# Performance work log

Measured on AMD Instinct MI355X. Metric: run time of the kernel, lower is better.

The kernel has to match this reference:

```python
import math
import jax, jax.numpy as jnp
import numpy as np

S, M, B, D, H = 256, 256, 8, 512, 8
HD = D // H
K = S + M  # key_len


def setup_inputs() -> dict:
    key = jax.random.key(0)
    ks = jax.random.split(key, 10)
    x = jax.random.normal(ks[0], (S, B, D), jnp.float32)
    memory = jax.random.normal(ks[1], (M, B, D), jnp.float32)
    rel_pos = jax.random.normal(ks[2], (K, D), jnp.float32)
    # causal mask: True means masked (key position after query position)
    q_pos = jnp.arange(S)[:, None] + M  # (S,1)
    k_pos = jnp.arange(K)[None, :]     # (1,K)
    attn_mask = jnp.broadcast_to(k_pos > q_pos, (B, S, K))
    scale = 1.0 / math.sqrt(D)
    Wq = jax.random.normal(ks[3], (D, D), jnp.float32) * scale
    Wk = jax.random.normal(ks[4], (D, D), jnp.float32) * scale
    Wv = jax.random.normal(ks[5], (D, D), jnp.float32) * scale
    Wr = jax.random.normal(ks[6], (D, D), jnp.float32) * scale
    Wo = jax.random.normal(ks[7], (D, D), jnp.float32) * scale
    u_bias = jax.random.normal(ks[8], (H, HD), jnp.float32) * 0.02
    v_bias = jax.random.normal(ks[9], (H, HD), jnp.float32) * 0.02
    return {"x": x, "memory": memory, "rel_pos": rel_pos, "attn_mask": attn_mask,
            "Wq": Wq, "Wk": Wk, "Wv": Wv, "Wr": Wr, "Wo": Wo,
            "u_bias": u_bias, "v_bias": v_bias}


def reference(x, memory, rel_pos, attn_mask, Wq, Wk, Wv, Wr, Wo, u_bias, v_bias):
    mem = jax.lax.stop_gradient(memory)
    kv = jnp.concatenate([mem, x], axis=0)  # (K, B, D)
    # projections (torch Linear: y = x @ W.T)
    q = (x @ Wq.T).reshape(S, B, H, HD).transpose(1, 2, 0, 3)   # (B,H,S,HD)
    k = (kv @ Wk.T).reshape(K, B, H, HD).transpose(1, 2, 0, 3)  # (B,H,K,HD)
    v = (kv @ Wv.T).reshape(K, B, H, HD).transpose(1, 2, 0, 3)  # (B,H,K,HD)
    r = (rel_pos[:K] @ Wr.T).reshape(K, H, HD)                  # (K,H,HD)
    # relative index gather
    q_pos = jnp.arange(S)[:, None] + M
    k_pos = jnp.arange(K)[None, :]
    rel_idx = jnp.clip(q_pos - k_pos, 0, K - 1)  # (S,K)
    r_qk = r[rel_idx]                            # (S,K,H,HD)
    qk = jnp.einsum('bhqd,bhkd->bhqk', q, k)
    qr = jnp.einsum('bhqd,qkhd->bhqk', q, r_qk)
    uk = jnp.einsum('hd,bhkd->bhk', u_bias, k)[:, :, None, :]
    vr = jnp.einsum('hd,qkhd->hqk', v_bias, r_qk)[None]
    scores = (qk + qr + uk + vr) / math.sqrt(HD)  # (B,H,S,K)
    scores = jnp.where(attn_mask[:, None, :, :], -jnp.inf, scores)
    weights = jax.nn.softmax(scores, axis=-1)
    y = jnp.einsum('bhqk,bhkd->bhqd', weights, v)
    y = y.transpose(2, 0, 1, 3).reshape(S, B, D)
    return y @ Wo.T
```

## Files before the change

### kernel.cpp

```cpp
#include <hip/hip_runtime.h>
#include <math.h>

constexpr int S_  = 256;
constexpr int Mm  = 256;
constexpr int Bb  = 8;
constexpr int Dd  = 512;
constexpr int Hh  = 8;
constexpr int HDd = 64;
constexpr int Kk  = 512;

typedef unsigned short u16;
typedef short bf16x8 __attribute__((ext_vector_type(8)));
typedef float f32x4  __attribute__((ext_vector_type(4)));

constexpr int LROW = 72;
constexpr int QSTR = 520;

__device__ __forceinline__ u16 f2b(float f) {
  union { float f; unsigned int u; } v; v.f = f;
  unsigned int u = v.u + 0x7fffu + ((v.u >> 16) & 1u);
  return (u16)(u >> 16);
}
__device__ __forceinline__ float b2f(u16 b) {
  union { unsigned int u; float f; } v; v.u = ((unsigned int)b) << 16;
  return v.f;
}

__device__ __forceinline__ void stage_bf16(u16* dst, const u16* __restrict__ src,
                                           int ld, int tid) {
  const int r = tid >> 3, c = (tid & 7) * 8;
  *(int4*)(dst + r * LROW + c)        = *(const int4*)(src + (size_t)r * ld + c);
  *(int4*)(dst + (r + 32) * LROW + c) = *(const int4*)(src + (size_t)(r + 32) * ld + c);
}
__device__ __forceinline__ void stage_f32(u16* dst, const float* __restrict__ src,
                                          int ld, int tid, int nrow32) {
  const int r = tid >> 3, c = (tid & 7) * 8;
  for (int hh = 0; hh < nrow32; ++hh) {
    const float4 a = *(const float4*)(src + (size_t)(r + 32 * hh) * ld + c);
    const float4 b = *(const float4*)(src + (size_t)(r + 32 * hh) * ld + c + 4);
    union { u16 u[8]; int4 v; } p;
    p.u[0] = f2b(a.x); p.u[1] = f2b(a.y); p.u[2] = f2b(a.z); p.u[3] = f2b(a.w);
    p.u[4] = f2b(b.x); p.u[5] = f2b(b.y); p.u[6] = f2b(b.z); p.u[7] = f2b(b.w);
    *(int4*)(dst + (r + 32 * hh) * LROW + c) = p.v;
  }
}

__device__ __forceinline__ void mfma_step(const u16* As, const u16* Bs,
                                          f32x4 (&acc)[4], int wave, int lane) {
  const int r16 = lane & 15, q8 = (lane >> 4) * 8;
#pragma unroll
  for (int ks = 0; ks < 64; ks += 32) {
    const bf16x8 a = *(const bf16x8*)(As + (wave * 16 + r16) * LROW + ks + q8);
#pragma unroll
    for (int nb = 0; nb < 4; ++nb) {
      const bf16x8 b = *(const bf16x8*)(Bs + (nb * 16 + r16) * LROW + ks + q8);
      acc[nb] = __builtin_amdgcn_mfma_f32_16x16x32_bf16(a, b, acc[nb], 0, 0, 0);
    }
  }
}

__global__ __launch_bounds__(256) void k_proj(const float* __restrict__ x,
                                              const float* __restrict__ mem,
                                              const float* __restrict__ rel,
                                              const float* __restrict__ Wq,
                                              const float* __restrict__ Wk,
                                              const float* __restrict__ Wv,
                                              const float* __restrict__ Wr,
                                              const float* __restrict__ ub,
                                              const float* __restrict__ vb,
                                              u16* __restrict__ qu,
                                              u16* __restrict__ qv,
                                              u16* __restrict__ kb,
                                              u16* __restrict__ vT,
                                              u16* __restrict__ rT) {
  __shared__ u16 As[128 * LROW], Bs[64 * LROW];
  const int tid = threadIdx.x, wave = tid >> 6, lane = tid & 63;
  const int r16 = lane & 15, q8 = (lane >> 4) * 8, rq = (lane >> 4) * 4;
  const int bid = blockIdx.x;
  int kind, mt, nt;
  const float *A, *B;
  if (bid < 128)      { kind = 0; int t = bid;       mt = t >> 3; nt = t & 7; B = Wq; }
  else if (bid < 384) { kind = 1; int t = bid - 128; mt = t >> 3; nt = t & 7; B = Wk; }
  else if (bid < 640) { kind = 2; int t = bid - 384; mt = t >> 3; nt = t & 7; B = Wv; }
  else                { kind = 3; int t = bid - 640; mt = t >> 3; nt = t & 7; B = Wr; }
  const int m0 = mt * 128, n0 = nt * 64;
  if (kind == 0)      A = x + (size_t)m0 * Dd;
  else if (kind == 3) A = rel + (size_t)m0 * Dd;
  else                A = (m0 < Mm * Bb) ? mem + (size_t)m0 * Dd
                                         : x + (size_t)(m0 - Mm * Bb) * Dd;
  B += (size_t)n0 * Dd;

  f32x4 acc[2][4];
#pragma unroll
  for (int mi = 0; mi < 2; ++mi)
#pragma unroll
    for (int nb = 0; nb < 4; ++nb) acc[mi][nb] = (f32x4){0.f, 0.f, 0.f, 0.f};

  for (int k0 = 0; k0 < Dd; k0 += 64) {
    stage_f32(As, A + k0, Dd, tid, 4);
    stage_f32(Bs, B + k0, Dd, tid, 2);
    __syncthreads();
#pragma unroll
    for (int ks = 0; ks < 64; ks += 32) {
      bf16x8 a[2];
#pragma unroll
      for (int mi = 0; mi < 2; ++mi)
        a[mi] = *(const bf16x8*)(As + (wave * 32 + mi * 16 + r16) * LROW + ks + q8);
#pragma unroll
      for (int nb = 0; nb < 4; ++nb) {
        const bf16x8 bb = *(const bf16x8*)(Bs + (nb * 16 + r16) * LROW + ks + q8);
#pragma unroll
        for (int mi = 0; mi < 2; ++mi)
          acc[mi][nb] = __builtin_amdgcn_mfma_f32_16x16x32_bf16(a[mi], bb, acc[mi][nb], 0, 0, 0);
      }
    }
    __syncthreads();
  }

  const int h = n0 >> 6;
  if (kind == 0) {
#pragma unroll
    for (int nb = 0; nb < 4; ++nb) {
      const int hd = nb * 16 + r16, n = n0 + hd;
      const float u = ub[n], v = vb[n];
#pragma unroll
      for (int mi = 0; mi < 2; ++mi)
#pragma unroll
        for (int r = 0; r < 4; ++r) {
          const int m = m0 + wave * 32 + mi * 16 + rq + r;
          const int s = m >> 3, b = m & 7;
          const size_t d = ((size_t)(b * Hh + h) * S_ + s) * HDd + hd;
          qu[d] = f2b(acc[mi][nb][r] + u);
          qv[d] = f2b(acc[mi][nb][r] + v);
        }
    }
  } else if (kind == 1) {
#pragma unroll
    for (int nb = 0; nb < 4; ++nb) {
      const int hd = nb * 16 + r16;
#pragma unroll
      for (int mi = 0; mi < 2; ++mi)
#pragma unroll
        for (int r = 0; r < 4; ++r) {
          const int m = m0 + wave * 32 + mi * 16 + rq + r;
          const int pos = m >> 3, b = m & 7;
          kb[((size_t)(b * Hh + h) * Kk + pos) * HDd + hd] = f2b(acc[mi][nb][r]);
        }
    }
  } else if (kind == 2) {
#pragma unroll
    for (int nb = 0; nb < 4; ++nb) {
      const int hd = nb * 16 + r16;
#pragma unroll
      for (int mi = 0; mi < 2; ++mi)
#pragma unroll
        for (int r = 0; r < 4; ++r) {
          const int m = m0 + wave * 32 + mi * 16 + rq + r;
          const int pos = m >> 3, b = m & 7;
          vT[((size_t)(b * Hh + h) * HDd + hd) * Kk + pos] = f2b(acc[mi][nb][r]);
        }
    }
  } else {
#pragma unroll
    for (int nb = 0; nb < 4; ++nb) {
      const int hd = nb * 16 + r16;
#pragma unroll
      for (int mi = 0; mi < 2; ++mi)
#pragma unroll
        for (int r = 0; r < 4; ++r) {
          const int j = m0 + wave * 32 + mi * 16 + rq + r;
          rT[((size_t)h * Kk + j) * HDd + hd] = f2b(acc[mi][nb][r]);
        }
    }
  }
}

__global__ __launch_bounds__(256) void k_attn(const u16* __restrict__ qu,
                                              const u16* __restrict__ qv,
                                              const u16* __restrict__ kb,
                                              const u16* __restrict__ vT,
                                              const u16* __restrict__ rT,
                                              u16* __restrict__ y) {
  extern __shared__ u16 lds[];
  u16* QRP = lds;
  u16* Bs  = lds + 64 * QSTR;
  const int tid = threadIdx.x, wave = tid >> 6, lane = tid & 63;
  const int q0 = blockIdx.x * 64, bh = blockIdx.y, h = bh & 7, b = bh >> 3;
  const int ntiles = (q0 >> 6) + 5;
  const int col = lane & 15, rq = (lane >> 4) * 4;
  const int r16 = lane & 15, q8 = (lane >> 4) * 8;

  const u16* qvp = qv + ((size_t)bh * S_ + q0 + wave * 16 + r16) * HDd;
  const bf16x8 av0 = *(const bf16x8*)(qvp + q8);
  const bf16x8 av1 = *(const bf16x8*)(qvp + 32 + q8);
#pragma unroll
  for (int jt = 0; jt < 8; ++jt) if (jt < ntiles) {
    stage_bf16(Bs, rT + ((size_t)h * Kk + jt * 64) * HDd, HDd, tid);
    __syncthreads();
    f32x4 c[4];
#pragma unroll
    for (int i = 0; i < 4; ++i) c[i] = (f32x4){0.f, 0.f, 0.f, 0.f};
#pragma unroll
    for (int ks = 0; ks < 64; ks += 32) {
      const bf16x8 a = ks ? av1 : av0;
#pragma unroll
      for (int nb = 0; nb < 4; ++nb) {
        const bf16x8 bb = *(const bf16x8*)(Bs + (nb * 16 + r16) * LROW + ks + q8);
        c[nb] = __builtin_amdgcn_mfma_f32_16x16x32_bf16(a, bb, c[nb], 0, 0, 0);
      }
    }
#pragma unroll
    for (int nb = 0; nb < 4; ++nb)
#pragma unroll
      for (int r = 0; r < 4; ++r)
        QRP[(wave * 16 + rq + r) * QSTR + jt * 64 + nb * 16 + col] = f2b(c[nb][r]);
    __syncthreads();
  }

  const u16* qup = qu + ((size_t)bh * S_ + q0 + wave * 16 + r16) * HDd;
  const bf16x8 au0 = *(const bf16x8*)(qup + q8);
  const bf16x8 au1 = *(const bf16x8*)(qup + 32 + q8);
  f32x4 sc[8][4];
#pragma unroll
  for (int kt = 0; kt < 8; ++kt) if (kt < ntiles) {
    stage_bf16(Bs, kb + ((size_t)bh * Kk + kt * 64) * HDd, HDd, tid);
    __syncthreads();
#pragma unroll
    for (int i = 0; i < 4; ++i) sc[kt][i] = (f32x4){0.f, 0.f, 0.f, 0.f};
#pragma unroll
    for (int ks = 0; ks < 64; ks += 32) {
      const bf16x8 a = ks ? au1 : au0;
#pragma unroll
      for (int nb = 0; nb < 4; ++nb) {
        const bf16x8 bb = *(const bf16x8*)(Bs + (nb * 16 + r16) * LROW + ks + q8);
        sc[kt][nb] = __builtin_amdgcn_mfma_f32_16x16x32_bf16(a, bb, sc[kt][nb], 0, 0, 0);
      }
    }
    __syncthreads();
  }

  float mx[4] = {-INFINITY, -INFINITY, -INFINITY, -INFINITY};
#pragma unroll
  for (int kt = 0; kt < 8; ++kt) if (kt < ntiles) {
#pragma unroll
    for (int nb = 0; nb < 4; ++nb) {
      const int kk = kt * 64 + nb * 16 + col;
#pragma unroll
      for (int r = 0; r < 4; ++r) {
        const int ql = wave * 16 + rq + r;
        const int q  = q0 + ql;
        float v;
        if (kk <= q + Mm) {
          const float qr = b2f(QRP[ql * QSTR + (q + Mm - kk)]);
          v = (sc[kt][nb][r] + qr) * 0.125f;
        } else {
          v = -INFINITY;
        }
        sc[kt][nb][r] = v;
        mx[r] = fmaxf(mx[r], v);
      }
    }
  }
#pragma unroll
  for (int r = 0; r < 4; ++r)
#pragma unroll
    for (int off = 1; off < 16; off <<= 1) mx[r] = fmaxf(mx[r], __shfl_xor(mx[r], off));
  float sum[4] = {0.f, 0.f, 0.f, 0.f};
#pragma unroll
  for (int kt = 0; kt < 8; ++kt) if (kt < ntiles)
#pragma unroll
    for (int nb = 0; nb < 4; ++nb)
#pragma unroll
      for (int r = 0; r < 4; ++r) {
        const float p = __expf(sc[kt][nb][r] - mx[r]);
        sc[kt][nb][r] = p;
        sum[r] += p;
      }
#pragma unroll
  for (int r = 0; r < 4; ++r)
#pragma unroll
    for (int off = 1; off < 16; off <<= 1) sum[r] += __shfl_xor(sum[r], off);
  float inv[4];
#pragma unroll
  for (int r = 0; r < 4; ++r) inv[r] = 1.0f / sum[r];

#pragma unroll
  for (int kt = 0; kt < 8; ++kt) if (kt < ntiles)
#pragma unroll
    for (int nb = 0; nb < 4; ++nb)
#pragma unroll
      for (int r = 0; r < 4; ++r)
        QRP[(wave * 16 + rq + r) * QSTR + kt * 64 + nb * 16 + col] =
            f2b(sc[kt][nb][r] * inv[r]);
  __syncthreads();

  f32x4 o[4];
#pragma unroll
  for (int i = 0; i < 4; ++i) o[i] = (f32x4){0.f, 0.f, 0.f, 0.f};
#pragma unroll
  for (int kt = 0; kt < 8; ++kt) if (kt < ntiles) {
    stage_bf16(Bs, vT + (size_t)bh * HDd * Kk + kt * 64, Kk, tid);
    __syncthreads();
#pragma unroll
    for (int ks = 0; ks < 64; ks += 32) {
      const bf16x8 a = *(const bf16x8*)(QRP + (wave * 16 + r16) * QSTR + kt * 64 + ks + q8);
#pragma unroll
      for (int nb = 0; nb < 4; ++nb) {
        const bf16x8 bv = *(const bf16x8*)(Bs + (nb * 16 + r16) * LROW + ks + q8);
        o[nb] = __builtin_amdgcn_mfma_f32_16x16x32_bf16(a, bv, o[nb], 0, 0, 0);
      }
    }
    __syncthreads();
  }
#pragma unroll
  for (int nb = 0; nb < 4; ++nb) {
    const int hd = nb * 16 + col;
#pragma unroll
    for (int r = 0; r < 4; ++r) {
      const int q = q0 + wave * 16 + rq + r;
      y[((size_t)q * Bb + b) * Dd + h * HDd + hd] = f2b(o[nb][r]);
    }
  }
}

__global__ __launch_bounds__(256) void k_out(const u16* __restrict__ y,
                                             const float* __restrict__ Wo,
                                             float* __restrict__ out) {
  __shared__ u16 As[64 * LROW], Bs[64 * LROW];
  const int tid = threadIdx.x, wave = tid >> 6, lane = tid & 63;
  const int n0 = blockIdx.x * 64, m0 = blockIdx.y * 64;
  f32x4 acc[4];
#pragma unroll
  for (int i = 0; i < 4; ++i) acc[i] = (f32x4){0.f, 0.f, 0.f, 0.f};
  for (int k0 = 0; k0 < Dd; k0 += 64) {
    stage_bf16(As, y + (size_t)m0 * Dd + k0, Dd, tid);
    stage_f32(Bs, Wo + (size_t)n0 * Dd + k0, Dd, tid, 2);
    __syncthreads();
    mfma_step(As, Bs, acc, wave, lane);
    __syncthreads();
  }
  const int col = lane & 15, rq = (lane >> 4) * 4;
#pragma unroll
  for (int nb = 0; nb < 4; ++nb) {
    const int n = n0 + nb * 16 + col;
#pragma unroll
    for (int r = 0; r < 4; ++r) {
      const int m = m0 + wave * 16 + rq + r;
      out[(size_t)m * Dd + n] = acc[nb][r];
    }
  }
}

extern "C" void kernel_launch(void* const* d_in, const int* in_sizes, int n_in,
                              void* d_out, int out_size, void* d_ws, size_t ws_size,
                              hipStream_t stream) {
  const float* x    = (const float*)d_in[0];
  const float* mem  = (const float*)d_in[1];
  const float* rel  = (const float*)d_in[2];
  const float* Wq = (const float*)d_in[4];
  const float* Wk = (const float*)d_in[5];
  const float* Wv = (const float*)d_in[6];
  const float* Wr = (const float*)d_in[7];
  const float* Wo = (const float*)d_in[8];
  const float* ub = (const float*)d_in[9];
  const float* vb = (const float*)d_in[10];
  float* out = (float*)d_out;

  u16* qu = (u16*)d_ws;
  u16* qv = qu + 1048576;
  u16* kb = qv + 1048576;
  u16* vT = kb + 2097152;
  u16* rT = vT + 2097152;
  u16* yb = rT + 262144;

  constexpr int ATTN_LDS = (64 * QSTR + 64 * LROW) * (int)sizeof(u16);
  (void)hipFuncSetAttribute((const void*)k_attn,
                            hipFuncAttributeMaxDynamicSharedMemorySize, ATTN_LDS);

  k_proj<<<dim3(672),   dim3(256), 0,        stream>>>(x, mem, rel, Wq, Wk, Wv, Wr,
                                                       ub, vb, qu, qv, kb, vT, rT);
  k_attn<<<dim3(4, 64), dim3(256), ATTN_LDS, stream>>>(qu, qv, kb, vT, rT, yb);
  k_out <<<dim3(8, 32), dim3(256), 0,        stream>>>(yb, Wo, out);
}
```

Before: 149.9 us.

## Double-buffer LDS staging in attention and output projection kernels

Merges the three attention phases (relative-position scores, QK scores, PV) into one 24-step loop. Each step prefetches the next tile into registers while computing on the current LDS buffer, halving barriers per tile. The output projection GEMM gets the same register-prefetch double buffering. The attention loop now always processes all 8 key tiles, dropping the causal tile-skipping, which adds work for early query blocks.

```diff
diff --git a/kernel.cpp b/kernel.cpp
--- a/kernel.cpp
+++ b/kernel.cpp
@@ -183,138 +183,159 @@
                                               u16* __restrict__ y) {
   extern __shared__ u16 lds[];
   u16* QRP = lds;
-  u16* Bs  = lds + 64 * QSTR;
+  u16* Bs0 = lds + 64 * QSTR;
+  u16* Bs1 = Bs0 + 64 * LROW;
   const int tid = threadIdx.x, wave = tid >> 6, lane = tid & 63;
   const int q0 = blockIdx.x * 64, bh = blockIdx.y, h = bh & 7, b = bh >> 3;
-  const int ntiles = (q0 >> 6) + 5;
-  const int col = lane & 15, rq = (lane >> 4) * 4;
-  const int r16 = lane & 15, q8 = (lane >> 4) * 8;
+  const int r16 = lane & 15, q8 = (lane >> 4) * 8, rq = (lane >> 4) * 4;
+  const int sr = tid >> 3, scg = (tid & 7) * 8;
 
   const u16* qvp = qv + ((size_t)bh * S_ + q0 + wave * 16 + r16) * HDd;
   const bf16x8 av0 = *(const bf16x8*)(qvp + q8);
   const bf16x8 av1 = *(const bf16x8*)(qvp + 32 + q8);
-#pragma unroll
-  for (int jt = 0; jt < 8; ++jt) if (jt < ntiles) {
-    stage_bf16(Bs, rT + ((size_t)h * Kk + jt * 64) * HDd, HDd, tid);
-    __syncthreads();
-    f32x4 c[4];
-#pragma unroll
-    for (int i = 0; i < 4; ++i) c[i] = (f32x4){0.f, 0.f, 0.f, 0.f};
-#pragma unroll
-    for (int ks = 0; ks < 64; ks += 32) {
-      const bf16x8 a = ks ? av1 : av0;
-#pragma unroll
-      for (int nb = 0; nb < 4; ++nb) {
-        const bf16x8 bb = *(const bf16x8*)(Bs + (nb * 16 + r16) * LROW + ks + q8);
-        c[nb] = __builtin_amdgcn_mfma_f32_16x16x32_bf16(a, bb, c[nb], 0, 0, 0);
-      }
-    }
-#pragma unroll
-    for (int nb = 0; nb < 4; ++nb)
-#pragma unroll
-      for (int r = 0; r < 4; ++r)
-        QRP[(wave * 16 + rq + r) * QSTR + jt * 64 + nb * 16 + col] = f2b(c[nb][r]);
-    __syncthreads();
-  }
-
   const u16* qup = qu + ((size_t)bh * S_ + q0 + wave * 16 + r16) * HDd;
   const bf16x8 au0 = *(const bf16x8*)(qup + q8);
   const bf16x8 au1 = *(const bf16x8*)(qup + 32 + q8);
+
+  const u16* rbase = rT + (size_t)h * Kk * HDd;
+  const u16* kbase = kb + (size_t)bh * Kk * HDd;
+  const u16* vbase = vT + (size_t)bh * HDd * Kk;
+
   f32x4 sc[8][4];
-#pragma unroll
-  for (int kt = 0; kt < 8; ++kt) if (kt < ntiles) {
-    stage_bf16(Bs, kb + ((size_t)bh * Kk + kt * 64) * HDd, HDd, tid);
+  f32x4 o[4];
+#pragma unroll
+  for (int nb = 0; nb < 4; ++nb) o[nb] = (f32x4){0.f, 0.f, 0.f, 0.f};
+  float mx[4]  = {-INFINITY, -INFINITY, -INFINITY, -INFINITY};
+
+  *(int4*)(Bs0 + sr * LROW + scg) =
+      *(const int4*)(rbase + (size_t)sr * HDd + scg);
+  *(int4*)(Bs0 + (sr + 32) * LROW + scg) =
+      *(const int4*)(rbase + (size_t)(sr + 32) * HDd + scg);
+  __syncthreads();
+
+#pragma unroll
+  for (int j = 0; j < 24; ++j) {
+    int4 L0, L1;
+    if (j < 23) {
+      const int jn = j + 1;
+      const u16* s;
+      int ld;
+      if (jn < 8)       { s = rbase + (size_t)(jn * 64) * HDd;       ld = HDd; }
+      else if (jn < 16) { s = kbase + (size_t)((jn - 8) * 64) * HDd; ld = HDd; }
+      else              { s = vbase + (jn - 16) * 64;                ld = Kk;  }
+      L0 = *(const int4*)(s + (size_t)sr * ld + scg);
+      L1 = *(const int4*)(s + (size_t)(sr + 32) * ld + scg);
+    }
+    const u16* buf = (j & 1) ? Bs1 : Bs0;
+
+    if (j < 8) {
+      f32x4 c4[4];
+#pragma unroll
+      for (int nb = 0; nb < 4; ++nb) c4[nb] = (f32x4){0.f, 0.f, 0.f, 0.f};
+#pragma unroll
+      for (int ks = 0; ks < 64; ks += 32) {
+        const bf16x8 a = ks ? av1 : av0;
+#pragma unroll
+        for (int nb = 0; nb < 4; ++nb) {
+          const bf16x8 bb = *(const bf16x8*)(buf + (nb * 16 + r16) * LROW + ks + q8);
+          c4[nb] = __builtin_amdgcn_mfma_f32_16x16x32_bf16(a, bb, c4[nb], 0, 0, 0);
+        }
+      }
+#pragma unroll
+      for (int nb = 0; nb < 4; ++nb)
+#pragma unroll
+        for (int r = 0; r < 4; ++r)
+          QRP[(wave * 16 + rq + r) * QSTR + j * 64 + nb * 16 + r16] = f2b(c4[nb][r]);
+    } else if (j < 16) {
+      const int t = j - 8;
+#pragma unroll
+      for (int nb = 0; nb < 4; ++nb) sc[t][nb] = (f32x4){0.f, 0.f, 0.f, 0.f};
+#pragma unroll
+      for (int ks = 0; ks < 64; ks += 32) {
+        const bf16x8 a = ks ? au1 : au0;
+#pragma unroll
+        for (int nb = 0; nb < 4; ++nb) {
+          const bf16x8 bb = *(const bf16x8*)(buf + (nb * 16 + r16) * LROW + ks + q8);
+          sc[t][nb] = __builtin_amdgcn_mfma_f32_16x16x32_bf16(a, bb, sc[t][nb], 0, 0, 0);
+        }
+      }
+      if (j == 15) {
+#pragma unroll
+        for (int kt = 0; kt < 8; ++kt)
+#pragma unroll
+          for (int nb = 0; nb < 4; ++nb) {
+            const int kk = kt * 64 + nb * 16 + r16;
+#pragma unroll
+            for (int r = 0; r < 4; ++r) {
+              const int ql = wave * 16 + rq + r;
+              const int q  = q0 + ql;
+              float v;
+              if (kk <= q + Mm) {
+                const float qr = b2f(QRP[ql * QSTR + (q + Mm - kk)]);
+                v = (sc[kt][nb][r] + qr) * 0.125f;
+              } else {
+                v = -INFINITY;
+              }
+              sc[kt][nb][r] = v;
+              mx[r] = fmaxf(mx[r], v);
+            }
+          }
+#pragma unroll
+        for (int r = 0; r < 4; ++r)
+#pragma unroll
+          for (int off = 1; off < 16; off <<= 1)
+            mx[r] = fmaxf(mx[r], __shfl_xor(mx[r], off));
+        float sum[4] = {0.f, 0.f, 0.f, 0.f};
+#pragma unroll
+        for (int kt = 0; kt < 8; ++kt)
+#pragma unroll
+          for (int nb = 0; nb < 4; ++nb)
+#pragma unroll
+            for (int r = 0; r < 4; ++r) {
+              const float p = __expf(sc[kt][nb][r] - mx[r]);
+              sc[kt][nb][r] = p;
+              sum[r] += p;
+            }
+#pragma unroll
+        for (int r = 0; r < 4; ++r)
+#pragma unroll
+          for (int off = 1; off < 16; off <<= 1) sum[r] += __shfl_xor(sum[r], off);
+        float inv[4];
+#pragma unroll
+        for (int r = 0; r < 4; ++r) inv[r] = 1.0f / sum[r];
+#pragma unroll
+        for (int kt = 0; kt < 8; ++kt)
+#pragma unroll
+          for (int nb = 0; nb < 4; ++nb)
+#pragma unroll
+            for (int r = 0; r < 4; ++r)
+              QRP[(wave * 16 + rq + r) * QSTR + kt * 64 + nb * 16 + r16] =
+                  f2b(sc[kt][nb][r] * inv[r]);
+      }
+    } else {
+      const int t = j - 16;
+#pragma unroll
+      for (int ks = 0; ks < 64; ks += 32) {
+        const bf16x8 a = *(const bf16x8*)(QRP + (wave * 16 + r16) * QSTR + t * 64 + ks + q8);
+#pragma unroll
+        for (int nb = 0; nb < 4; ++nb) {
+          const bf16x8 bb = *(const bf16x8*)(buf + (nb * 16 + r16) * LROW + ks + q8);
+          o[nb] = __builtin_amdgcn_mfma_f32_16x16x32_bf16(a, bb, o[nb], 0, 0, 0);
+        }
+      }
+    }
+
+    if (j < 23) {
+      u16* d = ((j + 1) & 1) ? Bs1 : Bs0;
+      *(int4*)(d + sr * LROW + scg)        = L0;
+      *(int4*)(d + (sr + 32) * LROW + scg) = L1;
+    }
     __syncthreads();
-#pragma unroll
-    for (int i = 0; i < 4; ++i) sc[kt][i] = (f32x4){0.f, 0.f, 0.f, 0.f};
-#pragma unroll
-    for (int ks = 0; ks < 64; ks += 32) {
-      const bf16x8 a = ks ? au1 : au0;
-#pragma unroll
-      for (int nb = 0; nb < 4; ++nb) {
-        const bf16x8 bb = *(const bf16x8*)(Bs + (nb * 16 + r16) * LROW + ks + q8);
-        sc[kt][nb] = __builtin_amdgcn_mfma_f32_16x16x32_bf16(a, bb, sc[kt][nb], 0, 0, 0);
-      }
-    }
-    __syncthreads();
-  }
-
-  float mx[4] = {-INFINITY, -INFINITY, -INFINITY, -INFINITY};
-#pragma unroll
-  for (int kt = 0; kt < 8; ++kt) if (kt < ntiles) {
-#pragma unroll
-    for (int nb = 0; nb < 4; ++nb) {
-      const int kk = kt * 64 + nb * 16 + col;
-#pragma unroll
-      for (int r = 0; r < 4; ++r) {
-        const int ql = wave * 16 + rq + r;
-        const int q  = q0 + ql;
-        float v;
-        if (kk <= q + Mm) {
-          const float qr = b2f(QRP[ql * QSTR + (q + Mm - kk)]);
-          v = (sc[kt][nb][r] + qr) * 0.125f;
-        } else {
-          v = -INFINITY;
-        }
-        sc[kt][nb][r] = v;
-        mx[r] = fmaxf(mx[r], v);
-      }
-    }
-  }
-#pragma unroll
-  for (int r = 0; r < 4; ++r)
-#pragma unroll
-    for (int off = 1; off < 16; off <<= 1) mx[r] = fmaxf(mx[r], __shfl_xor(mx[r], off));
-  float sum[4] = {0.f, 0.f, 0.f, 0.f};
-#pragma unroll
-  for (int kt = 0; kt < 8; ++kt) if (kt < ntiles)
-#pragma unroll
-    for (int nb = 0; nb < 4; ++nb)
-#pragma unroll
-      for (int r = 0; r < 4; ++r) {
-        const float p = __expf(sc[kt][nb][r] - mx[r]);
-        sc[kt][nb][r] = p;
-        sum[r] += p;
-      }
-#pragma unroll
-  for (int r = 0; r < 4; ++r)
-#pragma unroll
-    for (int off = 1; off < 16; off <<= 1) sum[r] += __shfl_xor(sum[r], off);
-  float inv[4];
-#pragma unroll
-  for (int r = 0; r < 4; ++r) inv[r] = 1.0f / sum[r];
-
-#pragma unroll
-  for (int kt = 0; kt < 8; ++kt) if (kt < ntiles)
-#pragma unroll
-    for (int nb = 0; nb < 4; ++nb)
-#pragma unroll
-      for (int r = 0; r < 4; ++r)
-        QRP[(wave * 16 + rq + r) * QSTR + kt * 64 + nb * 16 + col] =
-            f2b(sc[kt][nb][r] * inv[r]);
-  __syncthreads();
-
-  f32x4 o[4];
-#pragma unroll
-  for (int i = 0; i < 4; ++i) o[i] = (f32x4){0.f, 0.f, 0.f, 0.f};
-#pragma unroll
-  for (int kt = 0; kt < 8; ++kt) if (kt < ntiles) {
-    stage_bf16(Bs, vT + (size_t)bh * HDd * Kk + kt * 64, Kk, tid);
-    __syncthreads();
-#pragma unroll
-    for (int ks = 0; ks < 64; ks += 32) {
-      const bf16x8 a = *(const bf16x8*)(QRP + (wave * 16 + r16) * QSTR + kt * 64 + ks + q8);
-#pragma unroll
-      for (int nb = 0; nb < 4; ++nb) {
-        const bf16x8 bv = *(const bf16x8*)(Bs + (nb * 16 + r16) * LROW + ks + q8);
-        o[nb] = __builtin_amdgcn_mfma_f32_16x16x32_bf16(a, bv, o[nb], 0, 0, 0);
-      }
-    }
-    __syncthreads();
-  }
+  }
+
 #pragma unroll
   for (int nb = 0; nb < 4; ++nb) {
-    const int hd = nb * 16 + col;
+    const int hd = nb * 16 + r16;
 #pragma unroll
     for (int r = 0; r < 4; ++r) {
       const int q = q0 + wave * 16 + rq + r;
@@ -326,23 +347,55 @@
 __global__ __launch_bounds__(256) void k_out(const u16* __restrict__ y,
                                              const float* __restrict__ Wo,
                                              float* __restrict__ out) {
-  __shared__ u16 As[64 * LROW], Bs[64 * LROW];
+  __shared__ u16 As[2][64 * LROW], Bs[2][64 * LROW];
   const int tid = threadIdx.x, wave = tid >> 6, lane = tid & 63;
   const int n0 = blockIdx.x * 64, m0 = blockIdx.y * 64;
+  const int sr = tid >> 3, scg = (tid & 7) * 8;
+  const u16* Ay = y + (size_t)m0 * Dd;
+  const float* Bw = Wo + (size_t)n0 * Dd;
   f32x4 acc[4];
 #pragma unroll
   for (int i = 0; i < 4; ++i) acc[i] = (f32x4){0.f, 0.f, 0.f, 0.f};
-  for (int k0 = 0; k0 < Dd; k0 += 64) {
-    stage_bf16(As, y + (size_t)m0 * Dd + k0, Dd, tid);
-    stage_f32(Bs, Wo + (size_t)n0 * Dd + k0, Dd, tid, 2);
+
+  stage_bf16(As[0], Ay, Dd, tid);
+  stage_f32(Bs[0], Bw, Dd, tid, 2);
+  __syncthreads();
+
+#pragma unroll
+  for (int t = 0; t < 8; ++t) {
+    int4 La0, La1;
+    float4 f0, f1, f2, f3;
+    if (t < 7) {
+      const u16* s = Ay + (t + 1) * 64;
+      La0 = *(const int4*)(s + (size_t)sr * Dd + scg);
+      La1 = *(const int4*)(s + (size_t)(sr + 32) * Dd + scg);
+      const float* w = Bw + (t + 1) * 64;
+      f0 = *(const float4*)(w + (size_t)sr * Dd + scg);
+      f1 = *(const float4*)(w + (size_t)sr * Dd + scg + 4);
+      f2 = *(const float4*)(w + (size_t)(sr + 32) * Dd + scg);
+      f3 = *(const float4*)(w + (size_t)(sr + 32) * Dd + scg + 4);
+    }
+    mfma_step(As[t & 1], Bs[t & 1], acc, wave, lane);
+    if (t < 7) {
+      u16* da = As[(t + 1) & 1];
+      *(int4*)(da + sr * LROW + scg)        = La0;
+      *(int4*)(da + (sr + 32) * LROW + scg) = La1;
+      u16* db = Bs[(t + 1) & 1];
+      union { u16 u[8]; int4 v; } p;
+      p.u[0] = f2b(f0.x); p.u[1] = f2b(f0.y); p.u[2] = f2b(f0.z); p.u[3] = f2b(f0.w);
+      p.u[4] = f2b(f1.x); p.u[5] = f2b(f1.y); p.u[6] = f2b(f1.z); p.u[7] = f2b(f1.w);
+      *(int4*)(db + sr * LROW + scg) = p.v;
+      p.u[0] = f2b(f2.x); p.u[1] = f2b(f2.y); p.u[2] = f2b(f2.z); p.u[3] = f2b(f2.w);
+      p.u[4] = f2b(f3.x); p.u[5] = f2b(f3.y); p.u[6] = f2b(f3.z); p.u[7] = f2b(f3.w);
+      *(int4*)(db + (sr + 32) * LROW + scg) = p.v;
+    }
     __syncthreads();
-    mfma_step(As, Bs, acc, wave, lane);
-    __syncthreads();
-  }
-  const int col = lane & 15, rq = (lane >> 4) * 4;
+  }
+
+  const int r16 = lane & 15, rq = (lane >> 4) * 4;
 #pragma unroll
   for (int nb = 0; nb < 4; ++nb) {
-    const int n = n0 + nb * 16 + col;
+    const int n = n0 + nb * 16 + r16;
 #pragma unroll
     for (int r = 0; r < 4; ++r) {
       const int m = m0 + wave * 16 + rq + r;
@@ -373,7 +426,7 @@
   u16* rT = vT + 2097152;
   u16* yb = rT + 262144;
 
-  constexpr int ATTN_LDS = (64 * QSTR + 64 * LROW) * (int)sizeof(u16);
+  constexpr int ATTN_LDS = (64 * QSTR + 2 * 64 * LROW) * (int)sizeof(u16);
   (void)hipFuncSetAttribute((const void*)k_attn,
                             hipFuncAttributeMaxDynamicSharedMemorySize, ATTN_LDS);
 
```

Result: faster. 141.9 us (-5.3%).
